# Kernel tuning notes

Measured on AMD Instinct MI355X. Metric: run time of the kernel, lower is better.

The kernel has to match this reference:

```python
import jax, jax.numpy as jnp
import numpy as np

B, S, E = 2, 2048, 1024
H = 16
D = E // H  # head dim

def setup_inputs() -> dict:
    key = jax.random.key(0)
    ks = jax.random.split(key, 9)
    s = 1.0 / np.sqrt(E)
    return {
        "hidden_states": jax.random.normal(ks[0], (B, S, E), dtype=jnp.float32),
        "Wq": jax.random.normal(ks[1], (E, E), dtype=jnp.float32) * s,
        "bq": jnp.zeros((E,), jnp.float32),
        "Wk": jax.random.normal(ks[2], (E, E), dtype=jnp.float32) * s,
        "bk": jnp.zeros((E,), jnp.float32),
        "Wv": jax.random.normal(ks[3], (E, E), dtype=jnp.float32) * s,
        "bv": jnp.zeros((E,), jnp.float32),
        "Wo": jax.random.normal(ks[4], (E, E), dtype=jnp.float32) * s,
        "bo": jnp.zeros((E,), jnp.float32),
    }

def _split_heads(x):
    # [B,S,E] -> [B,H,S,D]
    b, s, _ = x.shape
    return x.reshape(b, s, H, D).transpose(0, 2, 1, 3)

def reference(hidden_states, Wq, bq, Wk, bk, Wv, bv, Wo, bo):
    q = _split_heads(hidden_states @ Wq + bq)  # [B,H,S,D]
    k = _split_heads(hidden_states @ Wk + bk)
    v = _split_heads(hidden_states @ Wv + bv)
    scores = jnp.einsum('bhqd,bhkd->bhqk', q, k) / jnp.sqrt(jnp.float32(D))
    probs = jax.nn.softmax(scores, axis=-1)  # [B,H,S,S]
    ctx = jnp.einsum('bhqk,bhkd->bhqd', probs, v)
    ctx = ctx.transpose(0, 2, 1, 3).reshape(hidden_states.shape[0], -1, E)
    out = ctx @ Wo + bo
    return out, probs
```

## Files before the change

kernel.cpp:

```cpp
#include <hip/hip_runtime.h>
#include <hip/hip_bf16.h>
#include <stdint.h>


typedef __attribute__((ext_vector_type(8))) short bf16x8;
typedef __attribute__((ext_vector_type(4))) short bf16x4v;
typedef __attribute__((ext_vector_type(4))) float f32x4;

#define DEV static __device__ __forceinline__

DEV short f2bs(float f) {
  union { __hip_bfloat16 b; short s; } u;
  u.b = __float2bfloat16(f);
  return u.s;
}
DEV f32x4 mfma16(bf16x8 a, bf16x8 b, f32x4 c) {
  return __builtin_amdgcn_mfma_f32_16x16x32_bf16(a, b, c, 0, 0, 0);
}
DEV float fexp2(float x) { return __builtin_amdgcn_exp2f(x); }
typedef const __attribute__((address_space(1))) void* gas1_t;
typedef __attribute__((address_space(3))) void* las3_t;
DEV void gload_lds16(const void* g, void* l) {
  __builtin_amdgcn_global_load_lds((gas1_t)(uintptr_t)g, (las3_t)(uint32_t)(uintptr_t)l,
                                   16, 0, 0);
}
#define WAIT_VMCNT(N) asm volatile("s_waitcnt vmcnt(" #N ")" ::: "memory")
#define WAIT_LGKM0() asm volatile("s_waitcnt lgkmcnt(0)" ::: "memory")
#define BARRIER() do { __builtin_amdgcn_s_barrier(); __builtin_amdgcn_sched_barrier(0); } while (0)

__global__ void cvt_all_kernel(const float* __restrict__ X,
                               const float* __restrict__ Wq, const float* __restrict__ Wk,
                               const float* __restrict__ Wv, const float* __restrict__ Wo,
                               short* __restrict__ Xb, short* __restrict__ Wt) {
  __shared__ short tile[64][68];
  int bx = blockIdx.x, t = threadIdx.x;
  if (bx < 2048) {
    size_t i = (size_t)bx * 256 + t;
    const float4* X4 = (const float4*)X;
    float4 a = X4[2 * i], c = X4[2 * i + 1];
    bf16x8 o;
    o[0] = f2bs(a.x); o[1] = f2bs(a.y); o[2] = f2bs(a.z); o[3] = f2bs(a.w);
    o[4] = f2bs(c.x); o[5] = f2bs(c.y); o[6] = f2bs(c.z); o[7] = f2bs(c.w);
    *(bf16x8*)(Xb + i * 8) = o;
    return;
  }
  int wb = bx - 2048;
  int mat = wb >> 8, rem = wb & 255;
  const float* W = mat == 0 ? Wq : mat == 1 ? Wk : mat == 2 ? Wv : Wo;
  int kb = (rem >> 4) * 64, nb = (rem & 15) * 64;
#pragma unroll
  for (int it = 0; it < 4; ++it) {
    int idx = it * 256 + t;
    int row = idx >> 4, c4 = (idx & 15) * 4;
    float4 v = *(const float4*)(W + (size_t)(kb + row) * 1024 + nb + c4);
    tile[row][c4 + 0] = f2bs(v.x); tile[row][c4 + 1] = f2bs(v.y);
    tile[row][c4 + 2] = f2bs(v.z); tile[row][c4 + 3] = f2bs(v.w);
  }
  __syncthreads();
#pragma unroll
  for (int it = 0; it < 4; ++it) {
    int idx = it * 256 + t;
    int rn = idx >> 4, c4 = (idx & 15) * 4;
    bf16x4v o;
    o[0] = tile[c4 + 0][rn]; o[1] = tile[c4 + 1][rn];
    o[2] = tile[c4 + 2][rn]; o[3] = tile[c4 + 3][rn];
    *(bf16x4v*)(Wt + (((size_t)mat) << 20) + (size_t)(nb + rn) * 1024 + kb + c4) = o;
  }
}

template <int MODE>
__global__ __launch_bounds__(256, 2)
void gemm_bt_kernel(const short* __restrict__ A, const short* __restrict__ Bt,
                    const float* __restrict__ bias0, const float* __restrict__ bias1,
                    const float* __restrict__ bias2,
                    short* __restrict__ o0, short* __restrict__ o1, short* __restrict__ o2,
                    float* __restrict__ fout) {
  __shared__ short As[128 * 32];
  __shared__ short Bs[128 * 32];
  const int m0 = blockIdx.x * 128, n0 = blockIdx.y * 128;
  const int t = threadIdx.x, w = t >> 6, l = t & 63, g = l >> 4, r = l & 15;
  const int wr = (w >> 1) * 64, wc = (w & 1) * 64;
  f32x4 acc[4][4] = {};
  for (int k0 = 0; k0 < 1024; k0 += 32) {
    gload_lds16(A + (size_t)(m0 + (t >> 2)) * 1024 + k0 + (t & 3) * 8, As + w * 512);
    gload_lds16(A + (size_t)(m0 + 64 + (t >> 2)) * 1024 + k0 + (t & 3) * 8, As + 2048 + w * 512);
    gload_lds16(Bt + (size_t)(n0 + (t >> 2)) * 1024 + k0 + (t & 3) * 8, Bs + w * 512);
    gload_lds16(Bt + (size_t)(n0 + 64 + (t >> 2)) * 1024 + k0 + (t & 3) * 8, Bs + 2048 + w * 512);
    __syncthreads();
    bf16x8 af[4], bfv[4];
#pragma unroll
    for (int i = 0; i < 4; i++) af[i] = *(const bf16x8*)(As + (wr + i * 16 + r) * 32 + g * 8);
#pragma unroll
    for (int j = 0; j < 4; j++) bfv[j] = *(const bf16x8*)(Bs + (wc + j * 16 + r) * 32 + g * 8);
#pragma unroll
    for (int i = 0; i < 4; i++)
#pragma unroll
      for (int j = 0; j < 4; j++) acc[i][j] = mfma16(af[i], bfv[j], acc[i][j]);
    __syncthreads();
  }
  if constexpr (MODE == 0) {
#pragma unroll
    for (int j = 0; j < 4; j++) {
      int ng = n0 + wc + j * 16 + r;
      int mat = ng >> 10, nn = ng & 1023, hh = nn >> 6, dd = nn & 63;
      const float* bp = mat == 0 ? bias0 : (mat == 1 ? bias1 : bias2);
      short* dst = mat == 0 ? o0 : (mat == 1 ? o1 : o2);
      float bv = bp[nn];
      float sc = (mat == 0) ? 0.18033688f : 1.0f;
#pragma unroll
      for (int i = 0; i < 4; i++) {
#pragma unroll
        for (int q = 0; q < 4; q++) {
          int m = m0 + wr + i * 16 + g * 4 + q;
          int bb = m >> 11, ss = m & 2047;
          dst[((size_t)(bb * 16 + hh) * 2048 + ss) * 64 + dd] = f2bs((acc[i][j][q] + bv) * sc);
        }
      }
    }
  } else {
#pragma unroll
    for (int i = 0; i < 4; i++)
#pragma unroll
      for (int q = 0; q < 4; q++) {
        int m = m0 + wr + i * 16 + g * 4 + q;
#pragma unroll
        for (int j = 0; j < 4; j++) {
          int ng = n0 + wc + j * 16 + r;
          fout[(size_t)m * 1024 + ng] = acc[i][j][q] + bias0[ng];
        }
      }
  }
}

__global__ __launch_bounds__(256, 3)
void attn_kernel(const short* __restrict__ Qm, const short* __restrict__ Km,
                 const short* __restrict__ Vm, float* __restrict__ probs,
                 short* __restrict__ ctx) {
  __shared__ short Ks[3][64 * 64];
  __shared__ short Vt[64 * 72];
  __shared__ short Ps[4][32 * 72];
  __shared__ float rls[128];
  const int f = blockIdx.x;
  const int wgid = (f & 7) * 64 + (f >> 3);
  const int bh = wgid >> 4, q0 = (wgid & 15) * 128;
  const int bb = bh >> 4, hh = bh & 15;
  const short* Qp = Qm + (size_t)bh * 2048 * 64;
  const short* Kp = Km + (size_t)bh * 2048 * 64;
  const short* Vp = Vm + (size_t)bh * 2048 * 64;
  float* Pp = probs + (size_t)bh * 2048 * 2048;
  const int t = threadIdx.x, w = t >> 6, l = t & 63, g = l >> 4, r = l & 15;
  const int lr = l >> 3, lc = l & 7;
  const int swz = lc ^ lr;

#define STAGE_K(kt_, buf_)                                                         \
  do {                                                                             \
    const short* src_ = Kp + (size_t)((kt_) * 64) * 64;                            \
    gload_lds16(src_ + (size_t)(w * 8 + lr) * 64 + swz * 8, Ks[buf_] + (w * 8) * 64); \
    gload_lds16(src_ + (size_t)(32 + w * 8 + lr) * 64 + swz * 8,                   \
                Ks[buf_] + (32 + w * 8) * 64);                                     \
  } while (0)

  short* Qs = &Ks[0][0];
#pragma unroll
  for (int it = 0; it < 4; ++it)
    gload_lds16(Qp + (size_t)(q0 + it * 32 + w * 8 + lr) * 64 + swz * 8,
                Qs + (it * 32 + w * 8) * 64);
  __syncthreads();
  bf16x8 qf[2][2];
#pragma unroll
  for (int qj = 0; qj < 2; qj++)
#pragma unroll
    for (int df = 0; df < 2; df++)
      qf[qj][df] = *(const bf16x8*)(Qs + (w * 32 + qj * 16 + r) * 64 + ((df * 4 + g) ^ (r & 7)) * 8);
  WAIT_LGKM0();
  BARRIER();

  float lrow[2] = {0.f, 0.f};
  STAGE_K(0, 0);
  for (int kt = 0; kt < 32; ++kt) {
    const int cur = kt % 3;
    if (kt < 31) {
      const int nxt = (kt + 1) % 3;
      STAGE_K(kt + 1, nxt);
      WAIT_VMCNT(2);
    } else {
      WAIT_VMCNT(0);
    }
    BARRIER();
    f32x4 st[4][2] = {};
#pragma unroll
    for (int df = 0; df < 2; ++df) {
      bf16x8 kf[4];
#pragma unroll
      for (int ni = 0; ni < 4; ni++)
        kf[ni] = *(const bf16x8*)(Ks[cur] + (ni * 16 + r) * 64 + ((df * 4 + g) ^ (r & 7)) * 8);
#pragma unroll
      for (int ni = 0; ni < 4; ni++)
#pragma unroll
        for (int qj = 0; qj < 2; qj++) st[ni][qj] = mfma16(kf[ni], qf[qj][df], st[ni][qj]);
    }
#pragma unroll
    for (int qj = 0; qj < 2; qj++) {
      float ssum = 0.f;
#pragma unroll
      for (int ni = 0; ni < 4; ni++)
#pragma unroll
        for (int q4 = 0; q4 < 4; q4++) ssum += fexp2(st[ni][qj][q4]);
      ssum += __shfl_xor(ssum, 16);
      ssum += __shfl_xor(ssum, 32);
      lrow[qj] += ssum;
    }
  }
  float rinv[2] = {1.0f / lrow[0], 1.0f / lrow[1]};
  if (g == 0) {
    rls[w * 32 + r] = rinv[0];
    rls[w * 32 + 16 + r] = rinv[1];
  }

  f32x4 cacc[2][4] = {};
  const int kp = (t >> 3) * 2, d0v = (t & 7) * 8, lcv = t & 7, kunit = t >> 5;
  STAGE_K(0, 0);
  for (int kt = 0; kt < 32; ++kt) {
    const int cur = kt % 3;
    bf16x8 v0 = *(const bf16x8*)(Vp + (size_t)(kt * 64 + kp) * 64 + d0v);
    bf16x8 v1 = *(const bf16x8*)(Vp + (size_t)(kt * 64 + kp + 1) * 64 + d0v);
    if (kt < 31) STAGE_K(kt + 1, (kt + 1) % 3);
    if (kt == 0) { WAIT_VMCNT(4); }
    else if (kt < 31) { WAIT_VMCNT(12); }
    else { WAIT_VMCNT(10); }
    BARRIER();
    f32x4 st[4][2] = {};
#pragma unroll
    for (int df = 0; df < 2; ++df) {
      bf16x8 kf[4];
#pragma unroll
      for (int ni = 0; ni < 4; ni++)
        kf[ni] = *(const bf16x8*)(Ks[cur] + (ni * 16 + r) * 64 + ((df * 4 + g) ^ (r & 7)) * 8);
#pragma unroll
      for (int ni = 0; ni < 4; ni++)
#pragma unroll
        for (int qj = 0; qj < 2; qj++) st[ni][qj] = mfma16(kf[ni], qf[qj][df], st[ni][qj]);
    }
#pragma unroll
    for (int ni = 0; ni < 4; ni++)
#pragma unroll
      for (int qj = 0; qj < 2; qj++) {
        bf16x4v pk;
#pragma unroll
        for (int q4 = 0; q4 < 4; q4++) {
          float pe = fexp2(st[ni][qj][q4]);
          st[ni][qj][q4] = pe;
          pk[q4] = f2bs(pe);
        }
        *(bf16x4v*)(&Ps[w][(qj * 16 + r) * 72 + ni * 16 + g * 4]) = pk;
      }
#pragma unroll
    for (int e = 0; e < 8; e++) {
      unsigned int pkv = (unsigned int)(unsigned short)v0[e] |
                         ((unsigned int)(unsigned short)v1[e] << 16);
      *(unsigned int*)(Vt + (d0v + e) * 72 + ((kunit ^ lcv) << 3) + (kp & 7)) = pkv;
    }
    WAIT_LGKM0();
    BARRIER();
#pragma unroll
    for (int kf4 = 0; kf4 < 2; ++kf4) {
      bf16x8 pa[2], vb[4];
#pragma unroll
      for (int qj = 0; qj < 2; qj++)
        pa[qj] = *(const bf16x8*)(&Ps[w][(qj * 16 + r) * 72 + kf4 * 32 + g * 8]);
#pragma unroll
      for (int nj = 0; nj < 4; nj++)
        vb[nj] = *(const bf16x8*)(Vt + (nj * 16 + r) * 72 +
                                  (((kf4 * 4 + g) ^ (nj * 2 + (r >> 3))) << 3));
#pragma unroll
      for (int qj = 0; qj < 2; qj++)
#pragma unroll
        for (int nj = 0; nj < 4; nj++) cacc[qj][nj] = mfma16(pa[qj], vb[nj], cacc[qj][nj]);
    }
#pragma unroll
    for (int ni = 0; ni < 4; ni++)
#pragma unroll
      for (int qj = 0; qj < 2; qj++) {
        f32x4 pr;
#pragma unroll
        for (int q4 = 0; q4 < 4; q4++) pr[q4] = st[ni][qj][q4] * rinv[qj];
        *(f32x4*)(Pp + (size_t)(q0 + w * 32 + qj * 16 + r) * 2048 + kt * 64 + ni * 16 + g * 4) = pr;
      }
  }
#pragma unroll
  for (int qj = 0; qj < 2; qj++)
#pragma unroll
    for (int nj = 0; nj < 4; nj++)
#pragma unroll
      for (int q4 = 0; q4 < 4; q4++) {
        int qt = w * 32 + qj * 16 + g * 4 + q4;
        float val = cacc[qj][nj][q4] * rls[qt];
        ctx[((size_t)(bb * 2048 + q0 + qt)) * 1024 + hh * 64 + nj * 16 + r] = f2bs(val);
      }
#undef STAGE_K
}

extern "C" void kernel_launch(void* const* d_in, const int* in_sizes, int n_in,
                              void* d_out, int out_size, void* d_ws, size_t ws_size,
                              hipStream_t stream) {
  (void)in_sizes; (void)n_in; (void)out_size; (void)ws_size;
  const float* X  = (const float*)d_in[0];
  const float* Wq = (const float*)d_in[1];
  const float* bq = (const float*)d_in[2];
  const float* Wk = (const float*)d_in[3];
  const float* bk = (const float*)d_in[4];
  const float* Wv = (const float*)d_in[5];
  const float* bv = (const float*)d_in[6];
  const float* Wo = (const float*)d_in[7];
  const float* bo = (const float*)d_in[8];
  float* out = (float*)d_out;
  float* probs = out + (size_t)2 * 2048 * 1024;

  short* Xb = (short*)d_ws;
  short* Wt = Xb + (size_t)4194304;
  short* Qb = Wt + (size_t)4194304;
  short* Kb = Qb + (size_t)4194304;
  short* Vb = Kb + (size_t)4194304;
  short* Cx = Vb + (size_t)4194304;

  cvt_all_kernel<<<3072, 256, 0, stream>>>(X, Wq, Wk, Wv, Wo, Xb, Wt);
  gemm_bt_kernel<0><<<dim3(32, 24), 256, 0, stream>>>(Xb, Wt, bq, bk, bv, Qb, Kb, Vb, nullptr);
  attn_kernel<<<512, 256, 0, stream>>>(Qb, Kb, Vb, probs, Cx);
  gemm_bt_kernel<1><<<dim3(32, 8), 256, 0, stream>>>(Cx, Wt + (size_t)3 * 1048576, bo,
                                                     nullptr, nullptr, nullptr, nullptr,
                                                     nullptr, out);
}
```

Baseline: 259.1 us.

## Halve attention query tile to 64 rows, double grid, add MFMA priority hints

Each attention workgroup now handles 64 query rows instead of 128 (16 per wave), so the grid doubles to 1024 blocks. K staging drops from triple to double buffering, which shrinks LDS enough to raise the occupancy target from 3 to 4 blocks per CU. The change also adds s_setprio around the MFMA sections, moves the probs store ahead of the PV MFMAs, and adds a barrier to the first pass. The aim is better latency hiding and load balance for this store-bound kernel, at the cost of reading K twice as often per query and having less MFMA work per K tile.

```diff
diff --git a/kernel.cpp b/kernel.cpp
--- a/kernel.cpp
+++ b/kernel.cpp
@@ -132,17 +132,17 @@
   }
 }
 
-__global__ __launch_bounds__(256, 3)
+__global__ __launch_bounds__(256, 4)
 void attn_kernel(const short* __restrict__ Qm, const short* __restrict__ Km,
                  const short* __restrict__ Vm, float* __restrict__ probs,
                  short* __restrict__ ctx) {
-  __shared__ short Ks[3][64 * 64];
+  __shared__ short Ks[2][64 * 64];
   __shared__ short Vt[64 * 72];
-  __shared__ short Ps[4][32 * 72];
-  __shared__ float rls[128];
+  __shared__ short Ps[4][16 * 72];
+  __shared__ float rls[64];
   const int f = blockIdx.x;
-  const int wgid = (f & 7) * 64 + (f >> 3);
-  const int bh = wgid >> 4, q0 = (wgid & 15) * 128;
+  const int wgid = (f & 7) * 128 + (f >> 3);
+  const int bh = wgid >> 5, q0 = (wgid & 31) * 64;
   const int bb = bh >> 4, hh = bh & 15;
   const short* Qp = Qm + (size_t)bh * 2048 * 64;
   const short* Kp = Km + (size_t)bh * 2048 * 64;
@@ -162,32 +162,30 @@
 
   short* Qs = &Ks[0][0];
 #pragma unroll
-  for (int it = 0; it < 4; ++it)
+  for (int it = 0; it < 2; ++it)
     gload_lds16(Qp + (size_t)(q0 + it * 32 + w * 8 + lr) * 64 + swz * 8,
                 Qs + (it * 32 + w * 8) * 64);
   __syncthreads();
-  bf16x8 qf[2][2];
-#pragma unroll
-  for (int qj = 0; qj < 2; qj++)
-#pragma unroll
-    for (int df = 0; df < 2; df++)
-      qf[qj][df] = *(const bf16x8*)(Qs + (w * 32 + qj * 16 + r) * 64 + ((df * 4 + g) ^ (r & 7)) * 8);
+  bf16x8 qf[2];
+#pragma unroll
+  for (int df = 0; df < 2; df++)
+    qf[df] = *(const bf16x8*)(Qs + (w * 16 + r) * 64 + ((df * 4 + g) ^ (r & 7)) * 8);
   WAIT_LGKM0();
   BARRIER();
 
-  float lrow[2] = {0.f, 0.f};
+  float lrow = 0.f;
   STAGE_K(0, 0);
   for (int kt = 0; kt < 32; ++kt) {
-    const int cur = kt % 3;
+    const int cur = kt & 1;
     if (kt < 31) {
-      const int nxt = (kt + 1) % 3;
-      STAGE_K(kt + 1, nxt);
+      STAGE_K(kt + 1, cur ^ 1);
       WAIT_VMCNT(2);
     } else {
       WAIT_VMCNT(0);
     }
     BARRIER();
-    f32x4 st[4][2] = {};
+    f32x4 st[4] = {};
+    __builtin_amdgcn_s_setprio(1);
 #pragma unroll
     for (int df = 0; df < 2; ++df) {
       bf16x8 kf[4];
@@ -195,41 +193,36 @@
       for (int ni = 0; ni < 4; ni++)
         kf[ni] = *(const bf16x8*)(Ks[cur] + (ni * 16 + r) * 64 + ((df * 4 + g) ^ (r & 7)) * 8);
 #pragma unroll
-      for (int ni = 0; ni < 4; ni++)
-#pragma unroll
-        for (int qj = 0; qj < 2; qj++) st[ni][qj] = mfma16(kf[ni], qf[qj][df], st[ni][qj]);
-    }
-#pragma unroll
-    for (int qj = 0; qj < 2; qj++) {
-      float ssum = 0.f;
-#pragma unroll
-      for (int ni = 0; ni < 4; ni++)
-#pragma unroll
-        for (int q4 = 0; q4 < 4; q4++) ssum += fexp2(st[ni][qj][q4]);
-      ssum += __shfl_xor(ssum, 16);
-      ssum += __shfl_xor(ssum, 32);
-      lrow[qj] += ssum;
-    }
-  }
-  float rinv[2] = {1.0f / lrow[0], 1.0f / lrow[1]};
-  if (g == 0) {
-    rls[w * 32 + r] = rinv[0];
-    rls[w * 32 + 16 + r] = rinv[1];
-  }
-
-  f32x4 cacc[2][4] = {};
+      for (int ni = 0; ni < 4; ni++) st[ni] = mfma16(kf[ni], qf[df], st[ni]);
+    }
+    __builtin_amdgcn_s_setprio(0);
+    float ssum = 0.f;
+#pragma unroll
+    for (int ni = 0; ni < 4; ni++)
+#pragma unroll
+      for (int q4 = 0; q4 < 4; q4++) ssum += fexp2(st[ni][q4]);
+    ssum += __shfl_xor(ssum, 16);
+    ssum += __shfl_xor(ssum, 32);
+    lrow += ssum;
+    BARRIER();
+  }
+  const float rinv = 1.0f / lrow;
+  if (g == 0) rls[w * 16 + r] = rinv;
+
+  f32x4 cacc[4] = {};
   const int kp = (t >> 3) * 2, d0v = (t & 7) * 8, lcv = t & 7, kunit = t >> 5;
   STAGE_K(0, 0);
   for (int kt = 0; kt < 32; ++kt) {
-    const int cur = kt % 3;
+    const int cur = kt & 1;
     bf16x8 v0 = *(const bf16x8*)(Vp + (size_t)(kt * 64 + kp) * 64 + d0v);
     bf16x8 v1 = *(const bf16x8*)(Vp + (size_t)(kt * 64 + kp + 1) * 64 + d0v);
-    if (kt < 31) STAGE_K(kt + 1, (kt + 1) % 3);
+    if (kt < 31) STAGE_K(kt + 1, cur ^ 1);
     if (kt == 0) { WAIT_VMCNT(4); }
-    else if (kt < 31) { WAIT_VMCNT(12); }
-    else { WAIT_VMCNT(10); }
+    else if (kt < 31) { WAIT_VMCNT(8); }
+    else { WAIT_VMCNT(6); }
     BARRIER();
-    f32x4 st[4][2] = {};
+    f32x4 st[4] = {};
+    __builtin_amdgcn_s_setprio(1);
 #pragma unroll
     for (int df = 0; df < 2; ++df) {
       bf16x8 kf[4];
@@ -237,23 +230,20 @@
       for (int ni = 0; ni < 4; ni++)
         kf[ni] = *(const bf16x8*)(Ks[cur] + (ni * 16 + r) * 64 + ((df * 4 + g) ^ (r & 7)) * 8);
 #pragma unroll
-      for (int ni = 0; ni < 4; ni++)
-#pragma unroll
-        for (int qj = 0; qj < 2; qj++) st[ni][qj] = mfma16(kf[ni], qf[qj][df], st[ni][qj]);
-    }
-#pragma unroll
-    for (int ni = 0; ni < 4; ni++)
-#pragma unroll
-      for (int qj = 0; qj < 2; qj++) {
-        bf16x4v pk;
-#pragma unroll
-        for (int q4 = 0; q4 < 4; q4++) {
-          float pe = fexp2(st[ni][qj][q4]);
-          st[ni][qj][q4] = pe;
-          pk[q4] = f2bs(pe);
-        }
-        *(bf16x4v*)(&Ps[w][(qj * 16 + r) * 72 + ni * 16 + g * 4]) = pk;
+      for (int ni = 0; ni < 4; ni++) st[ni] = mfma16(kf[ni], qf[df], st[ni]);
+    }
+    __builtin_amdgcn_s_setprio(0);
+#pragma unroll
+    for (int ni = 0; ni < 4; ni++) {
+      bf16x4v pk;
+#pragma unroll
+      for (int q4 = 0; q4 < 4; q4++) {
+        float pe = fexp2(st[ni][q4]);
+        st[ni][q4] = pe;
+        pk[q4] = f2bs(pe);
       }
+      *(bf16x4v*)(&Ps[w][r * 72 + ni * 16 + g * 4]) = pk;
+    }
 #pragma unroll
     for (int e = 0; e < 8; e++) {
       unsigned int pkv = (unsigned int)(unsigned short)v0[e] |
@@ -263,40 +253,34 @@
     WAIT_LGKM0();
     BARRIER();
 #pragma unroll
+    for (int ni = 0; ni < 4; ni++) {
+      f32x4 pr;
+#pragma unroll
+      for (int q4 = 0; q4 < 4; q4++) pr[q4] = st[ni][q4] * rinv;
+      *(f32x4*)(Pp + (size_t)(q0 + w * 16 + r) * 2048 + kt * 64 + ni * 16 + g * 4) = pr;
+    }
+    __builtin_amdgcn_s_setprio(1);
+#pragma unroll
     for (int kf4 = 0; kf4 < 2; ++kf4) {
-      bf16x8 pa[2], vb[4];
-#pragma unroll
-      for (int qj = 0; qj < 2; qj++)
-        pa[qj] = *(const bf16x8*)(&Ps[w][(qj * 16 + r) * 72 + kf4 * 32 + g * 8]);
+      bf16x8 pa, vb[4];
+      pa = *(const bf16x8*)(&Ps[w][r * 72 + kf4 * 32 + g * 8]);
 #pragma unroll
       for (int nj = 0; nj < 4; nj++)
         vb[nj] = *(const bf16x8*)(Vt + (nj * 16 + r) * 72 +
                                   (((kf4 * 4 + g) ^ (nj * 2 + (r >> 3))) << 3));
 #pragma unroll
-      for (int qj = 0; qj < 2; qj++)
-#pragma unroll
-        for (int nj = 0; nj < 4; nj++) cacc[qj][nj] = mfma16(pa[qj], vb[nj], cacc[qj][nj]);
-    }
-#pragma unroll
-    for (int ni = 0; ni < 4; ni++)
-#pragma unroll
-      for (int qj = 0; qj < 2; qj++) {
-        f32x4 pr;
-#pragma unroll
-        for (int q4 = 0; q4 < 4; q4++) pr[q4] = st[ni][qj][q4] * rinv[qj];
-        *(f32x4*)(Pp + (size_t)(q0 + w * 32 + qj * 16 + r) * 2048 + kt * 64 + ni * 16 + g * 4) = pr;
-      }
-  }
-#pragma unroll
-  for (int qj = 0; qj < 2; qj++)
-#pragma unroll
-    for (int nj = 0; nj < 4; nj++)
-#pragma unroll
-      for (int q4 = 0; q4 < 4; q4++) {
-        int qt = w * 32 + qj * 16 + g * 4 + q4;
-        float val = cacc[qj][nj][q4] * rls[qt];
-        ctx[((size_t)(bb * 2048 + q0 + qt)) * 1024 + hh * 64 + nj * 16 + r] = f2bs(val);
-      }
+      for (int nj = 0; nj < 4; nj++) cacc[nj] = mfma16(pa, vb[nj], cacc[nj]);
+    }
+    __builtin_amdgcn_s_setprio(0);
+  }
+#pragma unroll
+  for (int nj = 0; nj < 4; nj++)
+#pragma unroll
+    for (int q4 = 0; q4 < 4; q4++) {
+      int qt = w * 16 + g * 4 + q4;
+      float val = cacc[nj][q4] * rls[qt];
+      ctx[((size_t)(bb * 2048 + q0 + qt)) * 1024 + hh * 64 + nj * 16 + r] = f2bs(val);
+    }
 #undef STAGE_K
 }
 
@@ -325,7 +309,7 @@
 
   cvt_all_kernel<<<3072, 256, 0, stream>>>(X, Wq, Wk, Wv, Wo, Xb, Wt);
   gemm_bt_kernel<0><<<dim3(32, 24), 256, 0, stream>>>(Xb, Wt, bq, bk, bv, Qb, Kb, Vb, nullptr);
-  attn_kernel<<<512, 256, 0, stream>>>(Qb, Kb, Vb, probs, Cx);
+  attn_kernel<<<1024, 256, 0, stream>>>(Qb, Kb, Vb, probs, Cx);
   gemm_bt_kernel<1><<<dim3(32, 8), 256, 0, stream>>>(Cx, Wt + (size_t)3 * 1048576, bo,
                                                      nullptr, nullptr, nullptr, nullptr,
                                                      nullptr, out);
```

Measured after the change: 255.1 us. Within noise of the previous version (-1.5%).
